# Optimization experiments

Measured on AMD Instinct MI355X. Metric: run time of the kernel, lower is better.

Reference implementation:

```python
import jax, jax.numpy as jnp
import numpy as np

EMBED_DIM = 96
OUT_DIM = 192
HEADS = 2
HEAD_DIM = OUT_DIM // HEADS  # 96
STRIDE_Q = (1, 2, 2)
STRIDE_KV = (1, 8, 8)
SCALE = 1.0 / float(np.sqrt(HEAD_DIM))


def layer_norm(x, g, b, eps=1e-5):
    m = jnp.mean(x, -1, keepdims=True)
    v = jnp.mean(jnp.square(x - m), -1, keepdims=True)
    return (x - m) * jax.lax.rsqrt(v + eps) * g + b


def pool(x, thw, conv_w, g, b, stride):
    # x: [B, heads, N, d] with cls token at position 0; depthwise conv3d pool + LayerNorm(d)
    B, nh, N, d = x.shape
    T, H, W = thw
    cls_tok, rest = x[:, :, :1], x[:, :, 1:]
    rest = rest.transpose(0, 1, 3, 2).reshape(B * nh, d, T, H, W)
    rest = jax.lax.conv_general_dilated(
        rest, conv_w, stride, [(1, 1), (1, 1), (1, 1)],
        dimension_numbers=('NCDHW', 'OIDHW', 'NCDHW'), feature_group_count=d)
    T2, H2, W2 = rest.shape[2], rest.shape[3], rest.shape[4]
    rest = rest.reshape(B, nh, d, -1).transpose(0, 1, 3, 2)
    x = jnp.concatenate([cls_tok, rest], axis=2)
    return layer_norm(x, g, b), (T2, H2, W2)


def rel_idx(q_n, k_n):
    # decomposed relative-distance indices with q/k resolution ratio scaling
    q_r = max(k_n / q_n, 1.0)
    k_r = max(q_n / k_n, 1.0)
    d = (jnp.arange(q_n, dtype=jnp.float32)[:, None] * q_r
         - jnp.arange(k_n, dtype=jnp.float32)[None, :] * k_r + (k_n - 1) * k_r)
    return d.astype(jnp.int32)


def add_rel_pos(attn, q, q_thw, k_thw, rph, rpw, rpt):
    qt, qh, qw = q_thw
    kt, kh, kw = k_thw
    Rh = rph[rel_idx(qh, kh)]  # [qh, kh, d]
    Rw = rpw[rel_idx(qw, kw)]  # [qw, kw, d]
    Rt = rpt[rel_idx(qt, kt)]  # [qt, kt, d]
    B, nh, qN, d = q.shape
    r_q = q[:, :, 1:].reshape(B, nh, qt, qh, qw, d)
    rel_h = jnp.einsum('bythwc,hkc->bythwk', r_q, Rh)  # k = kh
    rel_w = jnp.einsum('bythwc,wkc->bythwk', r_q, Rw)  # k = kw
    rel_t = jnp.einsum('bythwc,tkc->bythwk', r_q, Rt)  # k = kt
    rel = (rel_t[..., :, None, None] + rel_h[..., None, :, None]
           + rel_w[..., None, None, :]).reshape(B, nh, qt * qh * qw, kt * kh * kw)
    return attn.at[:, :, 1:, 1:].add(rel)


def _forward(x, qkv_w, qkv_b, proj_w, proj_b, pq_w, nq_g, nq_b, pk_w, nk_g, nk_b,
             pv_w, nv_g, nv_b, rel_pos_h, rel_pos_w, rel_pos_t, thw):
    B, N, C = x.shape
    qkv = (x @ qkv_w.T + qkv_b).reshape(B, N, 3, HEADS, HEAD_DIM).transpose(2, 0, 3, 1, 4)
    q, k, v = qkv[0], qkv[1], qkv[2]  # each [B, heads, N, head_dim]
    k, k_thw = pool(k, thw, pk_w, nk_g, nk_b, STRIDE_KV)
    v, _ = pool(v, thw, pv_w, nv_g, nv_b, STRIDE_KV)
    q, q_thw = pool(q, thw, pq_w, nq_g, nq_b, STRIDE_Q)
    attn = jnp.einsum('bhqd,bhkd->bhqk', q * SCALE, k)
    attn = add_rel_pos(attn, q, q_thw, k_thw, rel_pos_h, rel_pos_w, rel_pos_t)
    attn = jax.nn.softmax(attn, axis=-1)
    out = jnp.einsum('bhqk,bhkd->bhqd', attn, v) + q  # residual_pool, with cls embed
    out = out.transpose(0, 2, 1, 3).reshape(B, -1, OUT_DIM)
    return out @ proj_w.T + proj_b


def setup_inputs() -> dict:
    key = jax.random.key(0)
    ks = jax.random.split(key, 10)
    T, H, W = 8, 56, 56
    N = 1 + T * H * W  # 25089
    B = 4
    std = 0.02
    return {
        'x': jax.random.normal(ks[0], (B, N, EMBED_DIM), jnp.float32),
        'qkv_w': jax.random.normal(ks[1], (3 * OUT_DIM, EMBED_DIM), jnp.float32) * std,
        'qkv_b': jnp.zeros((3 * OUT_DIM,), jnp.float32),
        'proj_w': jax.random.normal(ks[2], (OUT_DIM, OUT_DIM), jnp.float32) * std,
        'proj_b': jnp.zeros((OUT_DIM,), jnp.float32),
        'pq_w': jax.random.normal(ks[3], (HEAD_DIM, 1, 3, 3, 3), jnp.float32) * std,
        'nq_g': jnp.ones((HEAD_DIM,), jnp.float32),
        'nq_b': jnp.zeros((HEAD_DIM,), jnp.float32),
        'pk_w': jax.random.normal(ks[4], (HEAD_DIM, 1, 3, 3, 3), jnp.float32) * std,
        'nk_g': jnp.ones((HEAD_DIM,), jnp.float32),
        'nk_b': jnp.zeros((HEAD_DIM,), jnp.float32),
        'pv_w': jax.random.normal(ks[5], (HEAD_DIM, 1, 3, 3, 3), jnp.float32) * std,
        'nv_g': jnp.ones((HEAD_DIM,), jnp.float32),
        'nv_b': jnp.zeros((HEAD_DIM,), jnp.float32),
        'rel_pos_h': jax.random.normal(ks[6], (55, HEAD_DIM), jnp.float32) * std,
        'rel_pos_w': jax.random.normal(ks[7], (55, HEAD_DIM), jnp.float32) * std,
        'rel_pos_t': jax.random.normal(ks[8], (15, HEAD_DIM), jnp.float32) * std,
        'thw_t': 8, 'thw_h': 56, 'thw_w': 56,
    }


def reference(x, qkv_w, qkv_b, proj_w, proj_b, pq_w, nq_g, nq_b, pk_w, nk_g, nk_b,
              pv_w, nv_g, nv_b, rel_pos_h, rel_pos_w, rel_pos_t, thw_t, thw_h, thw_w):
    thw = (int(thw_t), int(thw_h), int(thw_w))
    return _forward(x, qkv_w, qkv_b, proj_w, proj_b, pq_w, nq_g, nq_b, pk_w, nk_g, nk_b,
                    pv_w, nv_g, nv_b, rel_pos_h, rel_pos_w, rel_pos_t, thw)
```

## Files before the change

kernel.cpp:

```cpp
#include <hip/hip_runtime.h>
#include <hip/hip_bf16.h>

typedef short short8 __attribute__((ext_vector_type(8)));
typedef float floatx4 __attribute__((ext_vector_type(4)));
typedef float floatx4v __attribute__((ext_vector_type(4)));

#define SCALE_F 0.10206207261596575f
#define TOKSTRIDE 401424

static __device__ __forceinline__ float b2f(unsigned short u){
  unsigned int v = ((unsigned int)u) << 16; float f;
  __builtin_memcpy(&f, &v, 4); return f;
}
static __device__ __forceinline__ unsigned short f2b(float f){
  __hip_bfloat16 h = __float2bfloat16(f);
  unsigned short u; __builtin_memcpy(&u, &h, 2); return u;
}
static __device__ __forceinline__ int map20(int i){
  return (i < 2) ? i : 7 + ((i-2)/3)*8 + ((i-2)%3);
}

struct ConvDesc {
  const void* src[17];
  long long off[17];
  int count[17];
};

__global__ __launch_bounds__(256) void k_convert(ConvDesc d, unsigned short* dst_base,
                                                 int* flagp, const unsigned int* xprobe)
{
  __shared__ int sflag;
  if (threadIdx.x < 64){
    unsigned int w = xprobe[1024 + threadIdx.x];
    int e = (w >> 7) & 0xFF;
    int pl = (e >= 90 && e <= 140) ? 1 : 0;
    unsigned long long m = __ballot(pl);
    if (threadIdx.x == 0){
      sflag = (__popcll(m) < 40) ? 1 : 0;
      if (blockIdx.x == 0 && blockIdx.y == 0) *flagp = sflag;
    }
  }
  __syncthreads();
  const int flag = sflag;
  const int t = blockIdx.y + 1;
  const int cnt = d.count[t];
  unsigned short* dst = dst_base + d.off[t];
  const float* sf = (const float*)d.src[t];
  const unsigned short* su = (const unsigned short*)d.src[t];
  for (int i = blockIdx.x*blockDim.x + threadIdx.x; i < cnt; i += gridDim.x*blockDim.x){
    dst[i] = flag ? f2b(sf[i]) : su[i];
  }
}

static __device__ __forceinline__ void load_x_frag(
    const void* xr_, int flag, size_t elem_off, short8& a0, short8& a1, short8& a2)
{
  if (flag){
    const float* xr = (const float*)xr_ + elem_off;
    floatx4v f0 = *(const floatx4v*)(xr),      f1 = *(const floatx4v*)(xr+4);
    floatx4v f2 = *(const floatx4v*)(xr+32),   f3 = *(const floatx4v*)(xr+36);
    floatx4v f4 = *(const floatx4v*)(xr+64),   f5 = *(const floatx4v*)(xr+68);
    #pragma unroll
    for (int j = 0; j < 4; ++j){
      a0[j] = (short)f2b(f0[j]); a0[j+4] = (short)f2b(f1[j]);
      a1[j] = (short)f2b(f2[j]); a1[j+4] = (short)f2b(f3[j]);
      a2[j] = (short)f2b(f4[j]); a2[j+4] = (short)f2b(f5[j]);
    }
  } else {
    const unsigned short* xr = (const unsigned short*)xr_ + elem_off;
    a0 = *(const short8*)(xr);
    a1 = *(const short8*)(xr + 32);
    a2 = *(const short8*)(xr + 64);
  }
}

__global__ __launch_bounds__(256) void k_qkv_q(
    const void* __restrict__ x, const unsigned short* __restrict__ w,
    const unsigned short* __restrict__ bias, unsigned short* __restrict__ qr,
    const int* __restrict__ flagp)
{
  const int flag = *flagp;
  const int lane = threadIdx.x & 63;
  const int wv = threadIdx.x >> 6;
  const int kq = (lane >> 4) * 8;
  const int col_l = lane & 15;
  const int m_base = blockIdx.x * 64 + wv * 16;

  int ma = m_base + col_l; if (ma > 100355) ma = 100355;
  short8 a0, a1, a2;
  load_x_frag(x, flag, (size_t)ma*96 + kq, a0, a1, a2);

  int bbase[4], ntok[4], mrow[4];
  #pragma unroll
  for (int r = 0; r < 4; ++r){
    int m = m_base + (lane >> 4)*4 + r;
    mrow[r] = m;
    int bb = m / 25089;
    ntok[r] = m - bb*25089;
    bbase[r] = bb*2;
  }

  #pragma unroll
  for (int ct = 0; ct < 12; ++ct){
    int col = ct*16 + col_l;
    const unsigned short* wrow = w + col*96 + kq;
    short8 b0 = *(const short8*)(wrow);
    short8 b1 = *(const short8*)(wrow + 32);
    short8 b2 = *(const short8*)(wrow + 64);
    float bv = b2f(bias[col]);
    floatx4 acc = {0.f,0.f,0.f,0.f};
    acc = __builtin_amdgcn_mfma_f32_16x16x32_bf16(a0, b0, acc, 0,0,0);
    acc = __builtin_amdgcn_mfma_f32_16x16x32_bf16(a1, b1, acc, 0,0,0);
    acc = __builtin_amdgcn_mfma_f32_16x16x32_bf16(a2, b2, acc, 0,0,0);
    const int head = ct / 6;
    const int dt6  = ct % 6;
    #pragma unroll
    for (int r = 0; r < 4; ++r){
      if (mrow[r] < 100356)
        qr[(size_t)((bbase[r]+head)*6 + dt6)*TOKSTRIDE + (size_t)ntok[r]*16 + col_l]
          = f2b(acc[r] + bv);
    }
  }
}

__global__ __launch_bounds__(256) void k_qkv_kv(
    const void* __restrict__ x, const unsigned short* __restrict__ w,
    const unsigned short* __restrict__ bias,
    unsigned short* __restrict__ kc, unsigned short* __restrict__ vc,
    unsigned short* __restrict__ kcls, unsigned short* __restrict__ vcls,
    const int* __restrict__ flagp)
{
  const int flag = *flagp;
  const int isv = blockIdx.y;
  const int lane = threadIdx.x & 63;
  const int wv = threadIdx.x >> 6;
  const int kq = (lane >> 4) * 8;
  const int quad = lane >> 4;
  const int col_l = lane & 15;
  const int rbase = blockIdx.x * 64 + wv * 16;

  int rhoA = rbase + col_l; if (rhoA > 12803) rhoA = 12803;
  int bA, nA;
  if (rhoA < 4){ bA = rhoA; nA = 0; }
  else {
    int rp = rhoA - 4;
    bA = rp / 3200; int rem = rp - bA*3200;
    int t = rem / 400; int s = rem - t*400;
    int ry = s / 20, rx = s - ry*20;
    nA = 1 + (t*56 + map20(ry))*56 + map20(rx);
  }
  short8 a0, a1, a2;
  load_x_frag(x, flag, ((size_t)bA*25089 + nA)*96 + kq, a0, a1, a2);

  int isCls[4], bI[4], baseI[4], valid[4];
  #pragma unroll
  for (int r = 0; r < 4; ++r){
    int rho = rbase + quad*4 + r;
    valid[r] = (rho < 12804);
    if (rho > 12803) rho = 12803;
    if (rho < 4){ isCls[r] = 1; bI[r] = rho; baseI[r] = 0; }
    else {
      int rp = rho - 4;
      int b = rp / 3200; int rem = rp - b*3200;
      int t = rem / 400; int s = rem - t*400;
      int ry = s / 20, rx = s - ry*20;
      isCls[r] = 0; bI[r] = b;
      baseI[r] = (((b*8 + t)*20 + ry)*20 + rx)*192;
    }
  }

  unsigned short* buf  = isv ? vc : kc;
  unsigned short* bufc = isv ? vcls : kcls;
  #pragma unroll
  for (int ct = 0; ct < 12; ++ct){
    const int col = 192 + (isv*12 + ct)*16 + col_l;
    const unsigned short* wrow = w + col*96 + kq;
    short8 b0 = *(const short8*)(wrow);
    short8 b1 = *(const short8*)(wrow + 32);
    short8 b2 = *(const short8*)(wrow + 64);
    float bv = b2f(bias[col]);
    floatx4 acc = {0.f,0.f,0.f,0.f};
    acc = __builtin_amdgcn_mfma_f32_16x16x32_bf16(a0, b0, acc, 0,0,0);
    acc = __builtin_amdgcn_mfma_f32_16x16x32_bf16(a1, b1, acc, 0,0,0);
    acc = __builtin_amdgcn_mfma_f32_16x16x32_bf16(a2, b2, acc, 0,0,0);
    const int head = ct / 6;
    const int dstat = (ct % 6) * 16;
    #pragma unroll
    for (int r = 0; r < 4; ++r){
      if (valid[r]){
        float o = acc[r] + bv;
        if (isCls[r]) bufc[(bI[r]*2 + head)*96 + dstat + col_l] = f2b(o);
        else          buf[baseI[r] + head*96 + dstat + col_l]   = f2b(o);
      }
    }
  }
}

__global__ __launch_bounds__(384) void k_poolq(
    const unsigned short* __restrict__ qr, const unsigned short* __restrict__ cw,
    const unsigned short* __restrict__ g, const unsigned short* __restrict__ bta,
    unsigned short* __restrict__ qp)
{
  __shared__ float wlds[27*96];
  __shared__ float gls[96], bls[96];
  __shared__ float ls1[29*12], ls2[29*12];
  __shared__ float lmean[29], linvs[29];

  const int y  = blockIdx.x;
  const int t  = blockIdx.y;
  const int bh = blockIdx.z;
  const int tid = threadIdx.x;
  const bool has_cls = (y == 0 && t == 0);

  for (int idx = tid; idx < 27*96; idx += 384){
    int tap = idx / 96, d = idx - tap*96;
    wlds[idx] = b2f(cw[d*27 + tap]);
  }
  for (int idx = tid; idx < 96; idx += 384){
    gls[idx] = b2f(g[idx]); bls[idx] = b2f(bta[idx]);
  }
  __syncthreads();

  const int x = tid / 12, dg = tid - x*12;
  const unsigned short* rowb = qr + (size_t)(bh*6 + (dg >> 1))*TOKSTRIDE + (dg & 1)*8;
  float val[8] = {0,0,0,0,0,0,0,0};

  if (x < 28){
    #pragma unroll
    for (int dt = 0; dt < 3; ++dt){
      int tt = t + dt - 1; if (tt < 0 || tt >= 8) continue;
      #pragma unroll
      for (int dy = 0; dy < 3; ++dy){
        int yy = 2*y + dy - 1; if (yy < 0 || yy >= 56) continue;
        #pragma unroll
        for (int dx = 0; dx < 3; ++dx){
          int xv = 2*x + dx - 1; if (xv < 0 || xv >= 56) continue;
          const int tap = (dt*3+dy)*3+dx;
          short8 v = *(const short8*)(rowb + (size_t)(1 + (tt*56 + yy)*56 + xv)*16);
          const float* wr = wlds + tap*96 + dg*8;
          #pragma unroll
          for (int j = 0; j < 8; ++j) val[j] += b2f((unsigned short)v[j]) * wr[j];
        }
      }
    }
    float s1 = 0.f, s2 = 0.f;
    #pragma unroll
    for (int j = 0; j < 8; ++j){ s1 += val[j]; s2 += val[j]*val[j]; }
    ls1[x*12+dg] = s1; ls2[x*12+dg] = s2;
  } else if (has_cls && tid >= 348 && tid < 360){
    int cdg = tid - 348;
    const unsigned short* rowc = qr + (size_t)(bh*6 + (cdg >> 1))*TOKSTRIDE + (cdg & 1)*8;
    short8 v = *(const short8*)(rowc);
    float s1 = 0.f, s2 = 0.f;
    #pragma unroll
    for (int j = 0; j < 8; ++j){ val[j] = b2f((unsigned short)v[j]); s1 += val[j]; s2 += val[j]*val[j]; }
    ls1[28*12+cdg] = s1; ls2[28*12+cdg] = s2;
  }
  __syncthreads();

  if (tid < 28 || (tid == 28 && has_cls)){
    float s1 = 0.f, s2 = 0.f;
    #pragma unroll
    for (int k = 0; k < 12; ++k){ s1 += ls1[tid*12+k]; s2 += ls2[tid*12+k]; }
    float mean = s1 * (1.f/96.f);
    float var  = s2 * (1.f/96.f) - mean*mean;
    lmean[tid] = mean; linvs[tid] = rsqrtf(var + 1e-5f);
  }
  __syncthreads();

  if (x < 28){
    float mean = lmean[x], inv = linvs[x];
    int tok = 1 + (t*28 + y)*28 + x;
    short8 o;
    #pragma unroll
    for (int j = 0; j < 8; ++j)
      o[j] = (short)f2b((val[j] - mean)*inv*gls[dg*8+j] + bls[dg*8+j]);
    *(short8*)(qp + ((size_t)bh*6273 + tok)*96 + dg*8) = o;
  } else if (has_cls && tid >= 348 && tid < 360){
    int cdg = tid - 348;
    float mean = lmean[28], inv = linvs[28];
    short8 o;
    #pragma unroll
    for (int j = 0; j < 8; ++j)
      o[j] = (short)f2b((val[j] - mean)*inv*gls[cdg*8+j] + bls[cdg*8+j]);
    *(short8*)(qp + (size_t)bh*6273*96 + cdg*8) = o;
  }
}

__global__ __launch_bounds__(128) void k_poolkv(
    const unsigned short* __restrict__ kc, const unsigned short* __restrict__ vc,
    const unsigned short* __restrict__ kcls, const unsigned short* __restrict__ vcls,
    const unsigned short* __restrict__ cwk, const unsigned short* __restrict__ gk, const unsigned short* __restrict__ bk,
    const unsigned short* __restrict__ cwv, const unsigned short* __restrict__ gv, const unsigned short* __restrict__ bv,
    unsigned short* __restrict__ kp, unsigned short* __restrict__ vt)
{
  const int bid = blockIdx.x;
  const int isv = blockIdx.y;
  const int bh = bid / 416; const int key = bid - bh*416;
  const int d = threadIdx.x;
  if (key >= 393){
    if (d < 96){
      if (isv == 0) kp[((size_t)bh*416 + key)*96 + d] = 0;
      else          vt[((size_t)bh*96 + d)*416 + key] = 0;
    }
    return;
  }
  const int b = bh >> 1, head = bh & 1;
  const unsigned short* buf  = isv ? vc : kc;
  const unsigned short* bufc = isv ? vcls : kcls;
  const unsigned short* cw = (isv == 0) ? cwk : cwv;
  const unsigned short* g  = (isv == 0) ? gk : gv;
  const unsigned short* bt = (isv == 0) ? bk : bv;
  float val = 0.f;
  if (d < 96){
    if (key == 0) val = b2f(bufc[bh*96 + d]);
    else {
      int s = key - 1; int t = s / 49; int r2 = s - t*49; int y = r2 / 7; int xx = r2 - y*7;
      const unsigned short* wr = cw + d*27;
      float sum = 0.f;
      #pragma unroll
      for (int dt = 0; dt < 3; ++dt){
        int tt = t + dt - 1; if (tt < 0 || tt >= 8) continue;
        #pragma unroll
        for (int dy = 0; dy < 3; ++dy){
          if (y == 0 && dy == 0) continue;
          int ry = (y == 0) ? (dy - 1) : 2 + 3*(y-1) + dy;
          #pragma unroll
          for (int dx = 0; dx < 3; ++dx){
            if (xx == 0 && dx == 0) continue;
            int rx = (xx == 0) ? (dx - 1) : 2 + 3*(xx-1) + dx;
            sum += b2f(buf[(((b*8 + tt)*20 + ry)*20 + rx)*192 + head*96 + d]) * b2f(wr[(dt*3+dy)*3+dx]);
          }
        }
      }
      val = sum;
    }
  }
  __shared__ float r1[128], r2s[128];
  r1[threadIdx.x] = (d < 96) ? val : 0.f;
  r2s[threadIdx.x] = (d < 96) ? val*val : 0.f;
  __syncthreads();
  for (int off = 64; off > 0; off >>= 1){
    if ((int)threadIdx.x < off){ r1[threadIdx.x] += r1[threadIdx.x+off]; r2s[threadIdx.x] += r2s[threadIdx.x+off]; }
    __syncthreads();
  }
  if (d < 96){
    float mean = r1[0] * (1.f/96.f);
    float var  = r2s[0] * (1.f/96.f) - mean*mean;
    float inv = rsqrtf(var + 1e-5f);
    float o = (val - mean)*inv*b2f(g[d]) + b2f(bt[d]);
    if (isv == 0) kp[((size_t)bh*416 + key)*96 + d] = f2b(o);
    else          vt[((size_t)bh*96 + d)*416 + key] = f2b(o);
  }
}

#define PSTR 424
__global__ __launch_bounds__(128) void k_attn(
    const unsigned short* __restrict__ qp, const unsigned short* __restrict__ kp,
    const unsigned short* __restrict__ vt,
    const unsigned short* __restrict__ rph, const unsigned short* __restrict__ rpw,
    const unsigned short* __restrict__ rpt,
    unsigned short* __restrict__ ao)
{
  __shared__ unsigned short P[16*PSTR];
  __shared__ float rel[16*24];
  __shared__ float mx_sh[2][16], sum_sh[2][16];

  const int bh = blockIdx.y;
  const int bb = bh >> 1, head = bh & 1;
  const int tid = threadIdx.x;
  const int lane = tid & 63;
  const int wv = tid >> 6;
  const int q0 = blockIdx.x * 16;

  const unsigned short* qbase = qp + (size_t)bh*6273*96;
  const unsigned short* kbase = kp + (size_t)bh*416*96;
  const unsigned short* vbase = vt + (size_t)bh*96*416;

  const int col = lane & 15;
  const int quad = lane >> 4;
  const int kq = quad * 8;
  const int t0 = wv * 13;

  short8 a0, a1, a2;
  {
    int qa = q0 + col; if (qa > 6272) qa = 6272;
    const unsigned short* qrow = qbase + (size_t)qa*96 + kq;
    a0 = *(const short8*)(qrow);
    a1 = *(const short8*)(qrow + 32);
    a2 = *(const short8*)(qrow + 64);
  }

  int yq4[4], xq4[4], tq4[4], livx[4], liv[4];
  #pragma unroll
  for (int r = 0; r < 4; ++r){
    int gq = q0 + quad*4 + r;
    liv[r]  = (gq >= 1);
    livx[r] = (gq >= 1 && gq <= 6272);
    int s = (gq >= 1) ? gq - 1 : 0;
    tq4[r] = s / 784; int r2 = s - tq4[r]*784; yq4[r] = r2 / 28; xq4[r] = r2 - yq4[r]*28;
  }

  #pragma unroll
  for (int cti = 0; cti < 4; ++cti){
    const int c = (wv*4 + cti)*16 + col;
    const unsigned short* rrow;
    if (c < 55)       rrow = rph + (size_t)c*96;
    else if (c < 110) rrow = rpw + (size_t)(c-55)*96;
    else { int ci = c-110; if (ci > 14) ci = 14; rrow = rpt + (size_t)ci*96; }
    rrow += kq;
    short8 b0 = *(const short8*)(rrow);
    short8 b1 = *(const short8*)(rrow + 32);
    short8 b2 = *(const short8*)(rrow + 64);
    floatx4 rc = {0.f,0.f,0.f,0.f};
    rc = __builtin_amdgcn_mfma_f32_16x16x32_bf16(a0, b0, rc, 0,0,0);
    rc = __builtin_amdgcn_mfma_f32_16x16x32_bf16(a1, b1, rc, 0,0,0);
    rc = __builtin_amdgcn_mfma_f32_16x16x32_bf16(a2, b2, rc, 0,0,0);
    #pragma unroll
    for (int r = 0; r < 4; ++r){
      if (!livx[r]) continue;
      const int m = quad*4 + r;
      if (c < 55){
        int u = yq4[r] + 24 - c;
        if (u >= 0 && u <= 24 && (u & 3) == 0) rel[m*24 + (u >> 2)] = rc[r];
      } else if (c < 110){
        int u = xq4[r] + 24 - (c - 55);
        if (u >= 0 && u <= 24 && (u & 3) == 0) rel[m*24 + 8 + (u >> 2)] = rc[r];
      } else if (c < 125){
        int u = tq4[r] + 7 - (c - 110);
        if (u >= 0 && u <= 7) rel[m*24 + 16 + u] = rc[r];
      }
    }
  }
  __syncthreads();

  const float* Tm[4];
  #pragma unroll
  for (int r = 0; r < 4; ++r) Tm[r] = rel + (quad*4 + r)*24;

  floatx4 acc[13];
  float mx[4] = {-1e30f,-1e30f,-1e30f,-1e30f};
  #pragma unroll
  for (int i = 0; i < 13; ++i){
    const int t = t0 + i;
    const unsigned short* krow = kbase + (size_t)(t*16 + col)*96 + kq;
    short8 b0 = *(const short8*)(krow);
    short8 b1 = *(const short8*)(krow + 32);
    short8 b2 = *(const short8*)(krow + 64);
    floatx4 a = {0.f,0.f,0.f,0.f};
    a = __builtin_amdgcn_mfma_f32_16x16x32_bf16(a0, b0, a, 0,0,0);
    a = __builtin_amdgcn_mfma_f32_16x16x32_bf16(a1, b1, a, 0,0,0);
    a = __builtin_amdgcn_mfma_f32_16x16x32_bf16(a2, b2, a, 0,0,0);
    const int key = t*16 + col;
    const bool validk = (key < 393);
    int kt = 0, ky = 0, kx = 0;
    if (key >= 1 && validk){
      int ks = key - 1; kt = ks / 49; int krm = ks - kt*49; ky = krm / 7; kx = krm - ky*7;
    }
    #pragma unroll
    for (int r = 0; r < 4; ++r){
      float s;
      if (!validk) s = -1e30f;
      else {
        s = a[r] * SCALE_F;
        if (key >= 1 && liv[r])
          s += Tm[r][ky] + Tm[r][8 + kx] + Tm[r][16 + kt];
      }
      a[r] = s;
      mx[r] = fmaxf(mx[r], s);
    }
    acc[i] = a;
  }
  #pragma unroll
  for (int r = 0; r < 4; ++r){
    #pragma unroll
    for (int o = 1; o < 16; o <<= 1) mx[r] = fmaxf(mx[r], __shfl_xor(mx[r], o, 64));
  }
  if (col == 0){
    #pragma unroll
    for (int r = 0; r < 4; ++r) mx_sh[wv][quad*4 + r] = mx[r];
  }
  __syncthreads();

  float M[4];
  #pragma unroll
  for (int r = 0; r < 4; ++r)
    M[r] = fmaxf(mx_sh[0][quad*4 + r], mx_sh[1][quad*4 + r]);
  float sum[4] = {0.f,0.f,0.f,0.f};
  #pragma unroll
  for (int i = 0; i < 13; ++i){
    #pragma unroll
    for (int r = 0; r < 4; ++r){
      float e = __expf(acc[i][r] - M[r]);
      acc[i][r] = e; sum[r] += e;
    }
  }
  #pragma unroll
  for (int r = 0; r < 4; ++r){
    #pragma unroll
    for (int o = 1; o < 16; o <<= 1) sum[r] += __shfl_xor(sum[r], o, 64);
  }
  if (col == 0){
    #pragma unroll
    for (int r = 0; r < 4; ++r) sum_sh[wv][quad*4 + r] = sum[r];
  }
  #pragma unroll
  for (int i = 0; i < 13; ++i){
    const int t = t0 + i;
    #pragma unroll
    for (int r = 0; r < 4; ++r)
      P[(quad*4 + r)*PSTR + t*16 + col] = f2b(acc[i][r]);
  }
  __syncthreads();

  float linv4[4];
  #pragma unroll
  for (int r = 0; r < 4; ++r)
    linv4[r] = 1.f / (sum_sh[0][quad*4 + r] + sum_sh[1][quad*4 + r]);

  short8 pf[13];
  #pragma unroll
  for (int s = 0; s < 13; ++s)
    pf[s] = *(const short8*)(P + col*PSTR + s*32 + kq);

  #pragma unroll
  for (int dti = 0; dti < 3; ++dti){
    const int dd = (wv*3 + dti)*16 + col;
    const unsigned short* vrow = vbase + (size_t)dd*416 + kq;
    floatx4 o = {0.f,0.f,0.f,0.f};
    #pragma unroll
    for (int s = 0; s < 13; ++s){
      short8 vf = *(const short8*)(vrow + s*32);
      o = __builtin_amdgcn_mfma_f32_16x16x32_bf16(pf[s], vf, o, 0,0,0);
    }
    #pragma unroll
    for (int r = 0; r < 4; ++r){
      int gq = q0 + quad*4 + r;
      if (gq <= 6272){
        float val = o[r] * linv4[r] + b2f(qbase[(size_t)gq*96 + dd]);
        ao[((size_t)bb*6273 + gq)*192 + head*96 + dd] = f2b(val);
      }
    }
  }
}

__global__ __launch_bounds__(256) void k_proj(
    const unsigned short* __restrict__ ao, const unsigned short* __restrict__ w,
    const unsigned short* __restrict__ bias, void* __restrict__ out, const int* __restrict__ flagp)
{
  const int flag = *flagp;
  const int lane = threadIdx.x & 63;
  const int wv = threadIdx.x >> 6;
  const int c = blockIdx.y*64 + wv*16 + (lane & 15);
  const int kq = (lane >> 4) * 8;
  short8 bfr[6];
  const unsigned short* wrow = w + c*192 + kq;
  #pragma unroll
  for (int s = 0; s < 6; ++s) bfr[s] = *(const short8*)(wrow + 32*s);
  float bv = b2f(bias[c]);
  const int m_base = blockIdx.x * 64;
  for (int i = 0; i < 4; ++i){
    int mt = m_base + i*16;
    int ma = mt + (lane & 15); if (ma > 25091) ma = 25091;
    const unsigned short* arow = ao + (size_t)ma*192 + kq;
    floatx4 acc = {0.f,0.f,0.f,0.f};
    #pragma unroll
    for (int s = 0; s < 6; ++s){
      short8 a = *(const short8*)(arow + 32*s);
      acc = __builtin_amdgcn_mfma_f32_16x16x32_bf16(a, bfr[s], acc, 0,0,0);
    }
    #pragma unroll
    for (int r = 0; r < 4; ++r){
      int m = mt + (lane >> 4)*4 + r;
      if (m < 25092){
        float o = acc[r] + bv;
        if (flag) ((float*)out)[(size_t)m*192 + c] = o;
        else      ((unsigned short*)out)[(size_t)m*192 + c] = f2b(o);
      }
    }
  }
}

extern "C" void kernel_launch(void* const* d_in, const int* in_sizes, int n_in,
                              void* d_out, int out_size, void* d_ws, size_t ws_size,
                              hipStream_t stream)
{
  char* p = (char*)d_ws;
  int* flagp = (int*)p; p += 16;
  unsigned short* conv = (unsigned short*)p;

  ConvDesc desc;
  long long cum = 0;
  for (int i = 0; i < 17; ++i){
    desc.src[i] = d_in[i];
    desc.off[i] = cum;
    desc.count[i] = in_sizes[i];
    cum += in_sizes[i];
  }
  p += (size_t)cum * 2;

  unsigned short* q_raw  = (unsigned short*)p; p += (size_t)19268352*2;
  unsigned short* kc     = (unsigned short*)p; p += (size_t)2457600*2;
  unsigned short* vc     = (unsigned short*)p; p += (size_t)2457600*2;
  unsigned short* kcls   = (unsigned short*)p; p += (size_t)768*2;
  unsigned short* vcls   = (unsigned short*)p; p += (size_t)768*2;
  unsigned short* q_pool = (unsigned short*)p; p += (size_t)4817664*2;
  unsigned short* k_pool = (unsigned short*)p; p += (size_t)319488*2;
  unsigned short* v_t    = (unsigned short*)p; p += (size_t)319488*2;
  unsigned short* a_out  = q_raw;

  const unsigned short* cqkv_w = conv + desc.off[1];
  const unsigned short* cqkv_b = conv + desc.off[2];
  const unsigned short* cproj_w= conv + desc.off[3];
  const unsigned short* cproj_b= conv + desc.off[4];
  const unsigned short* cpq_w  = conv + desc.off[5];
  const unsigned short* cnq_g  = conv + desc.off[6];
  const unsigned short* cnq_b  = conv + desc.off[7];
  const unsigned short* cpk_w  = conv + desc.off[8];
  const unsigned short* cnk_g  = conv + desc.off[9];
  const unsigned short* cnk_b  = conv + desc.off[10];
  const unsigned short* cpv_w  = conv + desc.off[11];
  const unsigned short* cnv_g  = conv + desc.off[12];
  const unsigned short* cnv_b  = conv + desc.off[13];
  const unsigned short* crph   = conv + desc.off[14];
  const unsigned short* crpw   = conv + desc.off[15];
  const unsigned short* crpt   = conv + desc.off[16];

  k_convert<<<dim3(16, 16), 256, 0, stream>>>(desc, conv, flagp, (const unsigned int*)d_in[0]);
  k_qkv_q <<<dim3(1569), 256, 0, stream>>>(d_in[0], cqkv_w, cqkv_b, q_raw, flagp);
  k_qkv_kv<<<dim3(201, 2), 256, 0, stream>>>(d_in[0], cqkv_w, cqkv_b, kc, vc, kcls, vcls, flagp);
  k_poolq<<<dim3(28, 8, 8), 384, 0, stream>>>(q_raw, cpq_w, cnq_g, cnq_b, q_pool);
  k_poolkv<<<dim3(8*416, 2), 128, 0, stream>>>(kc, vc, kcls, vcls, cpk_w, cnk_g, cnk_b, cpv_w, cnv_g, cnv_b, k_pool, v_t);
  k_attn <<<dim3(393, 8), 128, 0, stream>>>(q_pool, k_pool, v_t, crph, crpw, crpt, a_out);
  k_proj <<<dim3(393, 3), 256, 0, stream>>>(a_out, cproj_w, cproj_b, d_out, flagp);
}
```

Before: 277.8 us.

## Merge QKV launches and pooling launches into combined kernels, per-wave rel tables

The separate Q and KV projection kernels become one launch that dispatches on block index, and Q pooling plus K/V pooling are merged into one launch. K/V pooling now packs three key-units per 384-thread block. In attention, each wave computes its own full relative-position table instead of splitting it across waves, which removes a block barrier but doubles that table work. The aim is fewer launches and less serialization between small kernels, in exchange for larger LDS use and uneven block shapes.

```diff
diff --git a/kernel.cpp b/kernel.cpp
--- a/kernel.cpp
+++ b/kernel.cpp
@@ -74,283 +74,276 @@
   }
 }
 
-__global__ __launch_bounds__(256) void k_qkv_q(
+__global__ __launch_bounds__(256) void k_qkv(
     const void* __restrict__ x, const unsigned short* __restrict__ w,
     const unsigned short* __restrict__ bias, unsigned short* __restrict__ qr,
+    unsigned short* __restrict__ kc, unsigned short* __restrict__ vc,
+    unsigned short* __restrict__ kcls, unsigned short* __restrict__ vcls,
     const int* __restrict__ flagp)
 {
   const int flag = *flagp;
   const int lane = threadIdx.x & 63;
   const int wv = threadIdx.x >> 6;
   const int kq = (lane >> 4) * 8;
-  const int col_l = lane & 15;
-  const int m_base = blockIdx.x * 64 + wv * 16;
-
-  int ma = m_base + col_l; if (ma > 100355) ma = 100355;
-  short8 a0, a1, a2;
-  load_x_frag(x, flag, (size_t)ma*96 + kq, a0, a1, a2);
-
-  int bbase[4], ntok[4], mrow[4];
-  #pragma unroll
-  for (int r = 0; r < 4; ++r){
-    int m = m_base + (lane >> 4)*4 + r;
-    mrow[r] = m;
-    int bb = m / 25089;
-    ntok[r] = m - bb*25089;
-    bbase[r] = bb*2;
-  }
-
-  #pragma unroll
-  for (int ct = 0; ct < 12; ++ct){
-    int col = ct*16 + col_l;
-    const unsigned short* wrow = w + col*96 + kq;
-    short8 b0 = *(const short8*)(wrow);
-    short8 b1 = *(const short8*)(wrow + 32);
-    short8 b2 = *(const short8*)(wrow + 64);
-    float bv = b2f(bias[col]);
-    floatx4 acc = {0.f,0.f,0.f,0.f};
-    acc = __builtin_amdgcn_mfma_f32_16x16x32_bf16(a0, b0, acc, 0,0,0);
-    acc = __builtin_amdgcn_mfma_f32_16x16x32_bf16(a1, b1, acc, 0,0,0);
-    acc = __builtin_amdgcn_mfma_f32_16x16x32_bf16(a2, b2, acc, 0,0,0);
-    const int head = ct / 6;
-    const int dt6  = ct % 6;
-    #pragma unroll
-    for (int r = 0; r < 4; ++r){
-      if (mrow[r] < 100356)
-        qr[(size_t)((bbase[r]+head)*6 + dt6)*TOKSTRIDE + (size_t)ntok[r]*16 + col_l]
-          = f2b(acc[r] + bv);
-    }
-  }
-}
-
-__global__ __launch_bounds__(256) void k_qkv_kv(
-    const void* __restrict__ x, const unsigned short* __restrict__ w,
-    const unsigned short* __restrict__ bias,
-    unsigned short* __restrict__ kc, unsigned short* __restrict__ vc,
-    unsigned short* __restrict__ kcls, unsigned short* __restrict__ vcls,
-    const int* __restrict__ flagp)
-{
-  const int flag = *flagp;
-  const int isv = blockIdx.y;
-  const int lane = threadIdx.x & 63;
-  const int wv = threadIdx.x >> 6;
-  const int kq = (lane >> 4) * 8;
   const int quad = lane >> 4;
   const int col_l = lane & 15;
-  const int rbase = blockIdx.x * 64 + wv * 16;
-
-  int rhoA = rbase + col_l; if (rhoA > 12803) rhoA = 12803;
-  int bA, nA;
-  if (rhoA < 4){ bA = rhoA; nA = 0; }
-  else {
-    int rp = rhoA - 4;
-    bA = rp / 3200; int rem = rp - bA*3200;
-    int t = rem / 400; int s = rem - t*400;
-    int ry = s / 20, rx = s - ry*20;
-    nA = 1 + (t*56 + map20(ry))*56 + map20(rx);
-  }
-  short8 a0, a1, a2;
-  load_x_frag(x, flag, ((size_t)bA*25089 + nA)*96 + kq, a0, a1, a2);
-
-  int isCls[4], bI[4], baseI[4], valid[4];
-  #pragma unroll
-  for (int r = 0; r < 4; ++r){
-    int rho = rbase + quad*4 + r;
-    valid[r] = (rho < 12804);
-    if (rho > 12803) rho = 12803;
-    if (rho < 4){ isCls[r] = 1; bI[r] = rho; baseI[r] = 0; }
+
+  if (blockIdx.x < 1569){
+    const int m_base = blockIdx.x * 64 + wv * 16;
+    int ma = m_base + col_l; if (ma > 100355) ma = 100355;
+    short8 a0, a1, a2;
+    load_x_frag(x, flag, (size_t)ma*96 + kq, a0, a1, a2);
+
+    int bbase[4], ntok[4], mrow[4];
+    #pragma unroll
+    for (int r = 0; r < 4; ++r){
+      int m = m_base + quad*4 + r;
+      mrow[r] = m;
+      int bb = m / 25089;
+      ntok[r] = m - bb*25089;
+      bbase[r] = bb*2;
+    }
+
+    #pragma unroll
+    for (int ct = 0; ct < 12; ++ct){
+      int col = ct*16 + col_l;
+      const unsigned short* wrow = w + col*96 + kq;
+      short8 b0 = *(const short8*)(wrow);
+      short8 b1 = *(const short8*)(wrow + 32);
+      short8 b2 = *(const short8*)(wrow + 64);
+      float bv = b2f(bias[col]);
+      floatx4 acc = {0.f,0.f,0.f,0.f};
+      acc = __builtin_amdgcn_mfma_f32_16x16x32_bf16(a0, b0, acc, 0,0,0);
+      acc = __builtin_amdgcn_mfma_f32_16x16x32_bf16(a1, b1, acc, 0,0,0);
+      acc = __builtin_amdgcn_mfma_f32_16x16x32_bf16(a2, b2, acc, 0,0,0);
+      const int head = ct / 6;
+      const int dt6  = ct % 6;
+      #pragma unroll
+      for (int r = 0; r < 4; ++r){
+        if (mrow[r] < 100356)
+          qr[(size_t)((bbase[r]+head)*6 + dt6)*TOKSTRIDE + (size_t)ntok[r]*16 + col_l]
+            = f2b(acc[r] + bv);
+      }
+    }
+  } else {
+    const int id = blockIdx.x - 1569;
+    const int isv = id / 201;
+    const int bx = id - isv*201;
+    const int rbase = bx * 64 + wv * 16;
+
+    int rhoA = rbase + col_l; if (rhoA > 12803) rhoA = 12803;
+    int bA, nA;
+    if (rhoA < 4){ bA = rhoA; nA = 0; }
     else {
-      int rp = rho - 4;
-      int b = rp / 3200; int rem = rp - b*3200;
+      int rp = rhoA - 4;
+      bA = rp / 3200; int rem = rp - bA*3200;
       int t = rem / 400; int s = rem - t*400;
       int ry = s / 20, rx = s - ry*20;
-      isCls[r] = 0; bI[r] = b;
-      baseI[r] = (((b*8 + t)*20 + ry)*20 + rx)*192;
-    }
-  }
-
-  unsigned short* buf  = isv ? vc : kc;
-  unsigned short* bufc = isv ? vcls : kcls;
-  #pragma unroll
-  for (int ct = 0; ct < 12; ++ct){
-    const int col = 192 + (isv*12 + ct)*16 + col_l;
-    const unsigned short* wrow = w + col*96 + kq;
-    short8 b0 = *(const short8*)(wrow);
-    short8 b1 = *(const short8*)(wrow + 32);
-    short8 b2 = *(const short8*)(wrow + 64);
-    float bv = b2f(bias[col]);
-    floatx4 acc = {0.f,0.f,0.f,0.f};
-    acc = __builtin_amdgcn_mfma_f32_16x16x32_bf16(a0, b0, acc, 0,0,0);
-    acc = __builtin_amdgcn_mfma_f32_16x16x32_bf16(a1, b1, acc, 0,0,0);
-    acc = __builtin_amdgcn_mfma_f32_16x16x32_bf16(a2, b2, acc, 0,0,0);
-    const int head = ct / 6;
-    const int dstat = (ct % 6) * 16;
+      nA = 1 + (t*56 + map20(ry))*56 + map20(rx);
+    }
+    short8 a0, a1, a2;
+    load_x_frag(x, flag, ((size_t)bA*25089 + nA)*96 + kq, a0, a1, a2);
+
+    int isCls[4], bI[4], baseI[4], valid[4];
     #pragma unroll
     for (int r = 0; r < 4; ++r){
-      if (valid[r]){
-        float o = acc[r] + bv;
-        if (isCls[r]) bufc[(bI[r]*2 + head)*96 + dstat + col_l] = f2b(o);
-        else          buf[baseI[r] + head*96 + dstat + col_l]   = f2b(o);
-      }
-    }
-  }
-}
-
-__global__ __launch_bounds__(384) void k_poolq(
-    const unsigned short* __restrict__ qr, const unsigned short* __restrict__ cw,
-    const unsigned short* __restrict__ g, const unsigned short* __restrict__ bta,
-    unsigned short* __restrict__ qp)
-{
-  __shared__ float wlds[27*96];
-  __shared__ float gls[96], bls[96];
-  __shared__ float ls1[29*12], ls2[29*12];
-  __shared__ float lmean[29], linvs[29];
-
-  const int y  = blockIdx.x;
-  const int t  = blockIdx.y;
-  const int bh = blockIdx.z;
-  const int tid = threadIdx.x;
-  const bool has_cls = (y == 0 && t == 0);
-
-  for (int idx = tid; idx < 27*96; idx += 384){
-    int tap = idx / 96, d = idx - tap*96;
-    wlds[idx] = b2f(cw[d*27 + tap]);
-  }
-  for (int idx = tid; idx < 96; idx += 384){
-    gls[idx] = b2f(g[idx]); bls[idx] = b2f(bta[idx]);
-  }
-  __syncthreads();
-
-  const int x = tid / 12, dg = tid - x*12;
-  const unsigned short* rowb = qr + (size_t)(bh*6 + (dg >> 1))*TOKSTRIDE + (dg & 1)*8;
-  float val[8] = {0,0,0,0,0,0,0,0};
-
-  if (x < 28){
-    #pragma unroll
-    for (int dt = 0; dt < 3; ++dt){
-      int tt = t + dt - 1; if (tt < 0 || tt >= 8) continue;
-      #pragma unroll
-      for (int dy = 0; dy < 3; ++dy){
-        int yy = 2*y + dy - 1; if (yy < 0 || yy >= 56) continue;
-        #pragma unroll
-        for (int dx = 0; dx < 3; ++dx){
-          int xv = 2*x + dx - 1; if (xv < 0 || xv >= 56) continue;
-          const int tap = (dt*3+dy)*3+dx;
-          short8 v = *(const short8*)(rowb + (size_t)(1 + (tt*56 + yy)*56 + xv)*16);
-          const float* wr = wlds + tap*96 + dg*8;
-          #pragma unroll
-          for (int j = 0; j < 8; ++j) val[j] += b2f((unsigned short)v[j]) * wr[j];
+      int rho = rbase + quad*4 + r;
+      valid[r] = (rho < 12804);
+      if (rho > 12803) rho = 12803;
+      if (rho < 4){ isCls[r] = 1; bI[r] = rho; baseI[r] = 0; }
+      else {
+        int rp = rho - 4;
+        int b = rp / 3200; int rem = rp - b*3200;
+        int t = rem / 400; int s = rem - t*400;
+        int ry = s / 20, rx = s - ry*20;
+        isCls[r] = 0; bI[r] = b;
+        baseI[r] = (((b*8 + t)*20 + ry)*20 + rx)*192;
+      }
+    }
+
+    unsigned short* buf  = isv ? vc : kc;
+    unsigned short* bufc = isv ? vcls : kcls;
+    #pragma unroll
+    for (int ct = 0; ct < 12; ++ct){
+      const int col = 192 + (isv*12 + ct)*16 + col_l;
+      const unsigned short* wrow = w + col*96 + kq;
+      short8 b0 = *(const short8*)(wrow);
+      short8 b1 = *(const short8*)(wrow + 32);
+      short8 b2 = *(const short8*)(wrow + 64);
+      float bv = b2f(bias[col]);
+      floatx4 acc = {0.f,0.f,0.f,0.f};
+      acc = __builtin_amdgcn_mfma_f32_16x16x32_bf16(a0, b0, acc, 0,0,0);
+      acc = __builtin_amdgcn_mfma_f32_16x16x32_bf16(a1, b1, acc, 0,0,0);
+      acc = __builtin_amdgcn_mfma_f32_16x16x32_bf16(a2, b2, acc, 0,0,0);
+      const int head = ct / 6;
+      const int dstat = (ct % 6) * 16;
+      #pragma unroll
+      for (int r = 0; r < 4; ++r){
+        if (valid[r]){
+          float o = acc[r] + bv;
+          if (isCls[r]) bufc[(bI[r]*2 + head)*96 + dstat + col_l] = f2b(o);
+          else          buf[baseI[r] + head*96 + dstat + col_l]   = f2b(o);
         }
       }
     }
-    float s1 = 0.f, s2 = 0.f;
-    #pragma unroll
-    for (int j = 0; j < 8; ++j){ s1 += val[j]; s2 += val[j]*val[j]; }
-    ls1[x*12+dg] = s1; ls2[x*12+dg] = s2;
-  } else if (has_cls && tid >= 348 && tid < 360){
-    int cdg = tid - 348;
-    const unsigned short* rowc = qr + (size_t)(bh*6 + (cdg >> 1))*TOKSTRIDE + (cdg & 1)*8;
-    short8 v = *(const short8*)(rowc);
-    float s1 = 0.f, s2 = 0.f;
-    #pragma unroll
-    for (int j = 0; j < 8; ++j){ val[j] = b2f((unsigned short)v[j]); s1 += val[j]; s2 += val[j]*val[j]; }
-    ls1[28*12+cdg] = s1; ls2[28*12+cdg] = s2;
-  }
-  __syncthreads();
-
-  if (tid < 28 || (tid == 28 && has_cls)){
-    float s1 = 0.f, s2 = 0.f;
-    #pragma unroll
-    for (int k = 0; k < 12; ++k){ s1 += ls1[tid*12+k]; s2 += ls2[tid*12+k]; }
-    float mean = s1 * (1.f/96.f);
-    float var  = s2 * (1.f/96.f) - mean*mean;
-    lmean[tid] = mean; linvs[tid] = rsqrtf(var + 1e-5f);
-  }
-  __syncthreads();
-
-  if (x < 28){
-    float mean = lmean[x], inv = linvs[x];
-    int tok = 1 + (t*28 + y)*28 + x;
-    short8 o;
-    #pragma unroll
-    for (int j = 0; j < 8; ++j)
-      o[j] = (short)f2b((val[j] - mean)*inv*gls[dg*8+j] + bls[dg*8+j]);
-    *(short8*)(qp + ((size_t)bh*6273 + tok)*96 + dg*8) = o;
-  } else if (has_cls && tid >= 348 && tid < 360){
-    int cdg = tid - 348;
-    float mean = lmean[28], inv = linvs[28];
-    short8 o;
-    #pragma unroll
-    for (int j = 0; j < 8; ++j)
-      o[j] = (short)f2b((val[j] - mean)*inv*gls[cdg*8+j] + bls[cdg*8+j]);
-    *(short8*)(qp + (size_t)bh*6273*96 + cdg*8) = o;
-  }
-}
-
-__global__ __launch_bounds__(128) void k_poolkv(
+  }
+}
+
+__global__ __launch_bounds__(384) void k_pool(
+    const unsigned short* __restrict__ qr, const unsigned short* __restrict__ cwq,
+    const unsigned short* __restrict__ gq, const unsigned short* __restrict__ btaq,
+    unsigned short* __restrict__ qp,
     const unsigned short* __restrict__ kc, const unsigned short* __restrict__ vc,
     const unsigned short* __restrict__ kcls, const unsigned short* __restrict__ vcls,
     const unsigned short* __restrict__ cwk, const unsigned short* __restrict__ gk, const unsigned short* __restrict__ bk,
     const unsigned short* __restrict__ cwv, const unsigned short* __restrict__ gv, const unsigned short* __restrict__ bv,
     unsigned short* __restrict__ kp, unsigned short* __restrict__ vt)
 {
-  const int bid = blockIdx.x;
-  const int isv = blockIdx.y;
-  const int bh = bid / 416; const int key = bid - bh*416;
-  const int d = threadIdx.x;
-  if (key >= 393){
-    if (d < 96){
-      if (isv == 0) kp[((size_t)bh*416 + key)*96 + d] = 0;
-      else          vt[((size_t)bh*96 + d)*416 + key] = 0;
-    }
-    return;
-  }
-  const int b = bh >> 1, head = bh & 1;
-  const unsigned short* buf  = isv ? vc : kc;
-  const unsigned short* bufc = isv ? vcls : kcls;
-  const unsigned short* cw = (isv == 0) ? cwk : cwv;
-  const unsigned short* g  = (isv == 0) ? gk : gv;
-  const unsigned short* bt = (isv == 0) ? bk : bv;
-  float val = 0.f;
-  if (d < 96){
-    if (key == 0) val = b2f(bufc[bh*96 + d]);
-    else {
-      int s = key - 1; int t = s / 49; int r2 = s - t*49; int y = r2 / 7; int xx = r2 - y*7;
-      const unsigned short* wr = cw + d*27;
-      float sum = 0.f;
+  const int tid = threadIdx.x;
+  if (blockIdx.x < 1792){
+    __shared__ float wlds[27*96];
+    __shared__ float gls[96], bls[96];
+    __shared__ float ls1[29*12], ls2[29*12];
+    __shared__ float lmean[29], linvs[29];
+
+    const int bid = blockIdx.x;
+    const int y  = bid % 28;
+    const int t  = (bid / 28) % 8;
+    const int bh = bid / 224;
+    const bool has_cls = (y == 0 && t == 0);
+
+    for (int idx = tid; idx < 27*96; idx += 384){
+      int tap = idx / 96, d = idx - tap*96;
+      wlds[idx] = b2f(cwq[d*27 + tap]);
+    }
+    for (int idx = tid; idx < 96; idx += 384){
+      gls[idx] = b2f(gq[idx]); bls[idx] = b2f(btaq[idx]);
+    }
+    __syncthreads();
+
+    const int x = tid / 12, dg = tid - x*12;
+    const unsigned short* rowb = qr + (size_t)(bh*6 + (dg >> 1))*TOKSTRIDE + (dg & 1)*8;
+    float val[8] = {0,0,0,0,0,0,0,0};
+
+    if (x < 28){
       #pragma unroll
       for (int dt = 0; dt < 3; ++dt){
         int tt = t + dt - 1; if (tt < 0 || tt >= 8) continue;
         #pragma unroll
         for (int dy = 0; dy < 3; ++dy){
-          if (y == 0 && dy == 0) continue;
-          int ry = (y == 0) ? (dy - 1) : 2 + 3*(y-1) + dy;
+          int yy = 2*y + dy - 1; if (yy < 0 || yy >= 56) continue;
           #pragma unroll
           for (int dx = 0; dx < 3; ++dx){
-            if (xx == 0 && dx == 0) continue;
-            int rx = (xx == 0) ? (dx - 1) : 2 + 3*(xx-1) + dx;
-            sum += b2f(buf[(((b*8 + tt)*20 + ry)*20 + rx)*192 + head*96 + d]) * b2f(wr[(dt*3+dy)*3+dx]);
+            int xv = 2*x + dx - 1; if (xv < 0 || xv >= 56) continue;
+            const int tap = (dt*3+dy)*3+dx;
+            short8 v = *(const short8*)(rowb + (size_t)(1 + (tt*56 + yy)*56 + xv)*16);
+            const float* wr = wlds + tap*96 + dg*8;
+            #pragma unroll
+            for (int j = 0; j < 8; ++j) val[j] += b2f((unsigned short)v[j]) * wr[j];
           }
         }
       }
-      val = sum;
-    }
-  }
-  __shared__ float r1[128], r2s[128];
-  r1[threadIdx.x] = (d < 96) ? val : 0.f;
-  r2s[threadIdx.x] = (d < 96) ? val*val : 0.f;
-  __syncthreads();
-  for (int off = 64; off > 0; off >>= 1){
-    if ((int)threadIdx.x < off){ r1[threadIdx.x] += r1[threadIdx.x+off]; r2s[threadIdx.x] += r2s[threadIdx.x+off]; }
+      float s1 = 0.f, s2 = 0.f;
+      #pragma unroll
+      for (int j = 0; j < 8; ++j){ s1 += val[j]; s2 += val[j]*val[j]; }
+      ls1[x*12+dg] = s1; ls2[x*12+dg] = s2;
+    } else if (has_cls && tid >= 348 && tid < 360){
+      int cdg = tid - 348;
+      const unsigned short* rowc = qr + (size_t)(bh*6 + (cdg >> 1))*TOKSTRIDE + (cdg & 1)*8;
+      short8 v = *(const short8*)(rowc);
+      float s1 = 0.f, s2 = 0.f;
+      #pragma unroll
+      for (int j = 0; j < 8; ++j){ val[j] = b2f((unsigned short)v[j]); s1 += val[j]; s2 += val[j]*val[j]; }
+      ls1[28*12+cdg] = s1; ls2[28*12+cdg] = s2;
+    }
     __syncthreads();
-  }
-  if (d < 96){
-    float mean = r1[0] * (1.f/96.f);
-    float var  = r2s[0] * (1.f/96.f) - mean*mean;
-    float inv = rsqrtf(var + 1e-5f);
-    float o = (val - mean)*inv*b2f(g[d]) + b2f(bt[d]);
-    if (isv == 0) kp[((size_t)bh*416 + key)*96 + d] = f2b(o);
-    else          vt[((size_t)bh*96 + d)*416 + key] = f2b(o);
+
+    if (tid < 28 || (tid == 28 && has_cls)){
+      float s1 = 0.f, s2 = 0.f;
+      #pragma unroll
+      for (int k = 0; k < 12; ++k){ s1 += ls1[tid*12+k]; s2 += ls2[tid*12+k]; }
+      float mean = s1 * (1.f/96.f);
+      float var  = s2 * (1.f/96.f) - mean*mean;
+      lmean[tid] = mean; linvs[tid] = rsqrtf(var + 1e-5f);
+    }
+    __syncthreads();
+
+    if (x < 28){
+      float mean = lmean[x], inv = linvs[x];
+      int tok = 1 + (t*28 + y)*28 + x;
+      short8 o;
+      #pragma unroll
+      for (int j = 0; j < 8; ++j)
+        o[j] = (short)f2b((val[j] - mean)*inv*gls[dg*8+j] + bls[dg*8+j]);
+      *(short8*)(qp + ((size_t)bh*6273 + tok)*96 + dg*8) = o;
+    } else if (has_cls && tid >= 348 && tid < 360){
+      int cdg = tid - 348;
+      float mean = lmean[28], inv = linvs[28];
+      short8 o;
+      #pragma unroll
+      for (int j = 0; j < 8; ++j)
+        o[j] = (short)f2b((val[j] - mean)*inv*gls[cdg*8+j] + bls[cdg*8+j]);
+      *(short8*)(qp + (size_t)bh*6273*96 + cdg*8) = o;
+    }
+  } else {
+    __shared__ float r1[3][128], r2s[3][128];
+    const int unit = tid >> 7;
+    const int d = tid & 127;
+    const int u = (blockIdx.x - 1792)*3 + unit;
+    const bool live = (u < 6656);
+    int isv = 0, bh = 0, key = 0;
+    if (live){
+      isv = u / 3328; int rem = u - isv*3328;
+      bh = rem / 416; key = rem - bh*416;
+    }
+    const bool pad = (key >= 393);
+    const int b = bh >> 1, head = bh & 1;
+    const unsigned short* buf  = isv ? vc : kc;
+    const unsigned short* bufc = isv ? vcls : kcls;
+    const unsigned short* cw = (isv == 0) ? cwk : cwv;
+    const unsigned short* g  = (isv == 0) ? gk : gv;
+    const unsigned short* bt = (isv == 0) ? bk : bv;
+
+    float val = 0.f;
+    if (live && !pad && d < 96){
+      if (key == 0) val = b2f(bufc[bh*96 + d]);
+      else {
+        int s = key - 1; int t = s / 49; int r2 = s - t*49; int y = r2 / 7; int xx = r2 - y*7;
+        const unsigned short* wr = cw + d*27;
+        float sum = 0.f;
+        #pragma unroll
+        for (int dt = 0; dt < 3; ++dt){
+          int tt = t + dt - 1; if (tt < 0 || tt >= 8) continue;
+          #pragma unroll
+          for (int dy = 0; dy < 3; ++dy){
+            if (y == 0 && dy == 0) continue;
+            int ry = (y == 0) ? (dy - 1) : 2 + 3*(y-1) + dy;
+            #pragma unroll
+            for (int dx = 0; dx < 3; ++dx){
+              if (xx == 0 && dx == 0) continue;
+              int rx = (xx == 0) ? (dx - 1) : 2 + 3*(xx-1) + dx;
+              sum += b2f(buf[(((b*8 + tt)*20 + ry)*20 + rx)*192 + head*96 + d]) * b2f(wr[(dt*3+dy)*3+dx]);
+            }
+          }
+        }
+        val = sum;
+      }
+    }
+    r1[unit][d]  = (d < 96) ? val : 0.f;
+    r2s[unit][d] = (d < 96) ? val*val : 0.f;
+    __syncthreads();
+    for (int off = 64; off > 0; off >>= 1){
+      if (d < off){ r1[unit][d] += r1[unit][d+off]; r2s[unit][d] += r2s[unit][d+off]; }
+      __syncthreads();
+    }
+    if (live && d < 96){
+      float mean = r1[unit][0] * (1.f/96.f);
+      float var  = r2s[unit][0] * (1.f/96.f) - mean*mean;
+      float inv = rsqrtf(var + 1e-5f);
+      float o = pad ? 0.f : (val - mean)*inv*b2f(g[d]) + b2f(bt[d]);
+      if (isv == 0) kp[((size_t)bh*416 + key)*96 + d] = f2b(o);
+      else          vt[((size_t)bh*96 + d)*416 + key] = f2b(o);
+    }
   }
 }
 
@@ -363,7 +356,7 @@
     unsigned short* __restrict__ ao)
 {
   __shared__ unsigned short P[16*PSTR];
-  __shared__ float rel[16*24];
+  __shared__ float rel[2][16*24];
   __shared__ float mx_sh[2][16], sum_sh[2][16];
 
   const int bh = blockIdx.y;
@@ -401,9 +394,10 @@
     tq4[r] = s / 784; int r2 = s - tq4[r]*784; yq4[r] = r2 / 28; xq4[r] = r2 - yq4[r]*28;
   }
 
-  #pragma unroll
-  for (int cti = 0; cti < 4; ++cti){
-    const int c = (wv*4 + cti)*16 + col;
+  float* relw = &rel[wv][0];
+  #pragma unroll
+  for (int cti = 0; cti < 8; ++cti){
+    const int c = cti*16 + col;
     const unsigned short* rrow;
     if (c < 55)       rrow = rph + (size_t)c*96;
     else if (c < 110) rrow = rpw + (size_t)(c-55)*96;
@@ -422,21 +416,20 @@
       const int m = quad*4 + r;
       if (c < 55){
         int u = yq4[r] + 24 - c;
-        if (u >= 0 && u <= 24 && (u & 3) == 0) rel[m*24 + (u >> 2)] = rc[r];
+        if (u >= 0 && u <= 24 && (u & 3) == 0) relw[m*24 + (u >> 2)] = rc[r];
       } else if (c < 110){
         int u = xq4[r] + 24 - (c - 55);
-        if (u >= 0 && u <= 24 && (u & 3) == 0) rel[m*24 + 8 + (u >> 2)] = rc[r];
+        if (u >= 0 && u <= 24 && (u & 3) == 0) relw[m*24 + 8 + (u >> 2)] = rc[r];
       } else if (c < 125){
         int u = tq4[r] + 7 - (c - 110);
-        if (u >= 0 && u <= 7) rel[m*24 + 16 + u] = rc[r];
-      }
-    }
-  }
-  __syncthreads();
+        if (u >= 0 && u <= 7) relw[m*24 + 16 + u] = rc[r];
+      }
+    }
+  }
 
   const float* Tm[4];
   #pragma unroll
-  for (int r = 0; r < 4; ++r) Tm[r] = rel + (quad*4 + r)*24;
+  for (int r = 0; r < 4; ++r) Tm[r] = relw + (quad*4 + r)*24;
 
   floatx4 acc[13];
   float mx[4] = {-1e30f,-1e30f,-1e30f,-1e30f};
@@ -605,7 +598,7 @@
   unsigned short* kcls   = (unsigned short*)p; p += (size_t)768*2;
   unsigned short* vcls   = (unsigned short*)p; p += (size_t)768*2;
   unsigned short* q_pool = (unsigned short*)p; p += (size_t)4817664*2;
-  unsigned short* k_pool = (unsigned short*)p; p += (size_t)319488*2;
+  unsigned short* kp_buf = (unsigned short*)p; p += (size_t)319488*2;
   unsigned short* v_t    = (unsigned short*)p; p += (size_t)319488*2;
   unsigned short* a_out  = q_raw;
 
@@ -627,10 +620,10 @@
   const unsigned short* crpt   = conv + desc.off[16];
 
   k_convert<<<dim3(16, 16), 256, 0, stream>>>(desc, conv, flagp, (const unsigned int*)d_in[0]);
-  k_qkv_q <<<dim3(1569), 256, 0, stream>>>(d_in[0], cqkv_w, cqkv_b, q_raw, flagp);
-  k_qkv_kv<<<dim3(201, 2), 256, 0, stream>>>(d_in[0], cqkv_w, cqkv_b, kc, vc, kcls, vcls, flagp);
-  k_poolq<<<dim3(28, 8, 8), 384, 0, stream>>>(q_raw, cpq_w, cnq_g, cnq_b, q_pool);
-  k_poolkv<<<dim3(8*416, 2), 128, 0, stream>>>(kc, vc, kcls, vcls, cpk_w, cnk_g, cnk_b, cpv_w, cnv_g, cnv_b, k_pool, v_t);
-  k_attn <<<dim3(393, 8), 128, 0, stream>>>(q_pool, k_pool, v_t, crph, crpw, crpt, a_out);
+  k_qkv  <<<dim3(1971), 256, 0, stream>>>(d_in[0], cqkv_w, cqkv_b, q_raw, kc, vc, kcls, vcls, flagp);
+  k_pool <<<dim3(4011), 384, 0, stream>>>(q_raw, cpq_w, cnq_g, cnq_b, q_pool,
+                                          kc, vc, kcls, vcls,
+                                          cpk_w, cnk_g, cnk_b, cpv_w, cnv_g, cnv_b, kp_buf, v_t);
+  k_attn <<<dim3(393, 8), 128, 0, stream>>>(q_pool, kp_buf, v_t, crph, crpw, crpt, a_out);
   k_proj <<<dim3(393, 3), 256, 0, stream>>>(a_out, cproj_w, cproj_b, d_out, flagp);
 }
```

Measured after the change: 272.5 us. About the same (-1.9%).
